# Kernel optimization log

Hardware: AMD Instinct MI355X
Metric: run time of the kernel (lower is better)

## Reference

```python
import jax, jax.numpy as jnp
import numpy as np

S, B, D, H, WIN, L = 8192, 4, 512, 8, 64, 6
HD = D // H
EPS = 1e-5


def setup_inputs() -> dict:
    key = jax.random.key(0)
    ks = jax.random.split(key, 6)
    s = 0.02
    return {
        "src": jax.random.normal(ks[0], (S, B, D), jnp.float32),
        "Wqkv": jax.random.normal(ks[1], (L, 3 * D, D), jnp.float32) * s,
        "bqkv": jnp.zeros((L, 3 * D), jnp.float32),
        "Wo": jax.random.normal(ks[2], (L, D, D), jnp.float32) * s,
        "bo": jnp.zeros((L, D), jnp.float32),
        "W1": jax.random.normal(ks[3], (L, 4 * D, D), jnp.float32) * s,
        "bf1": jnp.zeros((L, 4 * D), jnp.float32),
        "W2": jax.random.normal(ks[4], (L, D, 4 * D), jnp.float32) * s,
        "bf2": jnp.zeros((L, D), jnp.float32),
        "g1": jnp.ones((L, D), jnp.float32),
        "beta1": jnp.zeros((L, D), jnp.float32),
        "g2": jnp.ones((L, D), jnp.float32),
        "beta2": jnp.zeros((L, D), jnp.float32),
    }


def layernorm(x, g, b):
    m = jnp.mean(x, axis=-1, keepdims=True)
    v = jnp.mean(jnp.square(x - m), axis=-1, keepdims=True)
    return (x - m) * jax.lax.rsqrt(v + EPS) * g + b


def _forward(src, Wqkv, bqkv, Wo, bo, W1, bf1, W2, bf2, g1, beta1, g2, beta2):
    NW = S // WIN
    scale = 1.0 / np.sqrt(HD)
    x = src
    for l in range(L):
        qkv = x @ Wqkv[l].T + bqkv[l]                      # (S,B,3D)
        q, k, v = jnp.split(qkv, 3, axis=-1)
        win = lambda t: t.reshape(NW, WIN, B, H, HD)       # (NW,W,B,H,hd)
        q = win(q) * scale
        k = win(k)
        v = win(v)
        att = jax.nn.softmax(jnp.einsum('nqbhd,nkbhd->nbhqk', q, k), axis=-1)
        o = jnp.einsum('nbhqk,nkbhd->nqbhd', att, v).reshape(S, B, D)
        o = o @ Wo[l].T + bo[l]
        x = layernorm(x + o, g1[l], beta1[l])
        # FFN with ReLU (hidden = 4*d_model)
        f = jax.nn.relu(x @ W1[l].T + bf1[l]) @ W2[l].T + bf2[l]
        x = layernorm(x + f, g2[l], beta2[l])
    return x


def reference(src, Wqkv, bqkv, Wo, bo, W1, bf1, W2, bf2, g1, beta1, g2, beta2):
    return _forward(src, Wqkv, bqkv, Wo, bo, W1, bf1, W2, bf2, g1, beta1, g2, beta2)
```

## Files before the change

kernel.cpp:

```cpp
#include <hip/hip_runtime.h>
#include <hip/hip_bf16.h>

typedef __bf16 bf16x8 __attribute__((ext_vector_type(8)));
typedef float f32x4 __attribute__((ext_vector_type(4)));

static constexpr int NT = 32768;
static constexpr int D_ = 512;
static constexpr int D3 = 1536;
static constexpr int DF = 2048;
static constexpr int L_ = 6;

#define AS1 __attribute__((address_space(1)))
#define AS3 __attribute__((address_space(3)))

__device__ __forceinline__ void gload_lds16(const void* g, void* l) {
  __builtin_amdgcn_global_load_lds((const AS1 void*)g, (AS3 void*)l, 16, 0, 0);
}

template<int K, int NTN, bool RELU>
__global__ __launch_bounds__(512, 2) void gemm256(
    const __hip_bfloat16* __restrict__ A,
    const __hip_bfloat16* __restrict__ W,
    const float* __restrict__ bias,
    __hip_bfloat16* __restrict__ Cout) {
  __shared__ __align__(16) char lds[131072];
  const int t = threadIdx.x;
  const int l = t & 63, w = t >> 6;
  const int lrow = l & 15, lhi = l >> 4;
  const int wr = w >> 2, wc = w & 3;

  const int lin = blockIdx.x;
  const int wg = (lin & 7) * ((int)gridDim.x >> 3) + (lin >> 3);
  const int tm0 = (wg / NTN) * 256, tn0 = (wg % NTN) * 256;

  constexpr int NKT = K / 64;
  constexpr int NIT = NKT / 2;
  constexpr int N = NTN * 256;

  const int srow = t >> 3;
  const int sun = t & 7;

  auto stage = [&](int buf, int reg, const __hip_bfloat16* P, int grow0, int tile) {
    const int kb = tile * 64;
    char* dst = lds + (buf * 4 + reg) * 16384 + w * 1024;
#pragma unroll
    for (int pass = 0; pass < 2; ++pass) {
      int rl = pass * 64 + srow;
      int u = sun ^ (rl & 7);
      gload_lds16(P + (size_t)(grow0 + rl) * K + kb + u * 8, dst + pass * 8192);
    }
  };
  auto rdA = [&](int buf, int m, int ks) -> bf16x8 {
    int r = m * 16 + lrow;
    return *(const bf16x8*)(lds + (buf * 4 + wr) * 16384 + r * 128 +
                            (((ks * 4 + lhi) ^ (r & 7)) << 4));
  };
  auto rdB = [&](int buf, int n, int ks) -> bf16x8 {
    int r = (wc & 1) * 64 + n * 16 + lrow;
    return *(const bf16x8*)(lds + (buf * 4 + 2 + (wc >> 1)) * 16384 + r * 128 +
                            (((ks * 4 + lhi) ^ (r & 7)) << 4));
  };

  f32x4 acc[8][4] = {};
  bf16x8 bfrag[4][2], afrag[2][2];

  stage(0, 2, W, tn0, 0);
  stage(0, 3, W, tn0 + 128, 0);
  stage(0, 0, A, tm0, 0);
  stage(0, 1, A, tm0 + 128, 0);
  stage(1, 2, W, tn0, 1);
  stage(1, 3, W, tn0 + 128, 1);
  asm volatile("s_waitcnt vmcnt(4)" ::: "memory");
  __builtin_amdgcn_s_barrier();

#define GPHASE(BUF, MB, RB, STG, VMS)                                       \
  {                                                                          \
    if (RB) {                                                                \
      _Pragma("unroll") for (int n = 0; n < 4; ++n)                          \
          _Pragma("unroll") for (int ks = 0; ks < 2; ++ks)                   \
              bfrag[n][ks] = rdB(BUF, n, ks);                                \
    }                                                                        \
    _Pragma("unroll") for (int ks = 0; ks < 2; ++ks) {                       \
      afrag[0][ks] = rdA(BUF, MB, ks);                                       \
      afrag[1][ks] = rdA(BUF, MB + 1, ks);                                   \
    }                                                                        \
    STG;                                                                     \
    VMS;                                                                     \
    __builtin_amdgcn_sched_barrier(0);                                       \
    __builtin_amdgcn_s_barrier();                                            \
    asm volatile("s_waitcnt lgkmcnt(0)" ::: "memory");                       \
    __builtin_amdgcn_sched_barrier(0);                                       \
    __builtin_amdgcn_s_setprio(1);                                           \
    _Pragma("unroll") for (int n = 0; n < 4; ++n)                            \
        _Pragma("unroll") for (int ks = 0; ks < 2; ++ks) {                   \
      acc[MB][n] = __builtin_amdgcn_mfma_f32_16x16x32_bf16(                  \
          afrag[0][ks], bfrag[n][ks], acc[MB][n], 0, 0, 0);                  \
      acc[MB + 1][n] = __builtin_amdgcn_mfma_f32_16x16x32_bf16(              \
          afrag[1][ks], bfrag[n][ks], acc[MB + 1][n], 0, 0, 0);              \
    }                                                                        \
    __builtin_amdgcn_s_setprio(0);                                           \
    __builtin_amdgcn_sched_barrier(0);                                       \
    __builtin_amdgcn_s_barrier();                                            \
  }

#define VM_CNT                                              \
  if (more) {                                               \
    asm volatile("s_waitcnt vmcnt(4)" ::: "memory");        \
  } else {                                                  \
    asm volatile("s_waitcnt vmcnt(0)" ::: "memory");        \
  }

  for (int it = 0; it < NIT; ++it) {
    const int t0 = 2 * it, t1 = 2 * it + 1;
    const bool more = (it + 1 < NIT);
    GPHASE(0, 0, 1, { stage(1, 0, A, tm0, t1); stage(1, 1, A, tm0 + 128, t1); }, );
    GPHASE(0, 2, 0, { if (more) stage(0, 2, W, tn0, t0 + 2); }, );
    GPHASE(0, 4, 0, { if (more) stage(0, 3, W, tn0 + 128, t0 + 2); }, );
    GPHASE(0, 6, 0, , VM_CNT);
    GPHASE(1, 0, 1, { if (more) stage(0, 0, A, tm0, t0 + 2); }, );
    GPHASE(1, 2, 0, { if (more) stage(0, 1, A, tm0 + 128, t0 + 2); }, );
    GPHASE(1, 4, 0, { if (more) stage(1, 2, W, tn0, t1 + 2); }, );
    GPHASE(1, 6, 0, { if (more) stage(1, 3, W, tn0 + 128, t1 + 2); }, VM_CNT);
  }
#undef GPHASE
#undef VM_CNT

  char* ep = lds + w * 16384;
#pragma unroll
  for (int n = 0; n < 4; ++n) {
    float bv = bias[tn0 + wc * 64 + n * 16 + lrow];
#pragma unroll
    for (int m = 0; m < 8; ++m)
#pragma unroll
      for (int j = 0; j < 4; ++j) {
        float v = acc[m][n][j] + bv;
        if (RELU) v = fmaxf(v, 0.f);
        int row = m * 16 + lhi * 4 + j;
        int col = n * 16 + lrow;
        *(__hip_bfloat16*)(ep + row * 128 + (((col >> 3) ^ (row & 7)) << 4) +
                           (col & 7) * 2) = __float2bfloat16(v);
      }
  }
  __builtin_amdgcn_sched_barrier(0);
  const int er = l >> 3, ec = l & 7;
#pragma unroll
  for (int p = 0; p < 16; ++p) {
    int r = p * 8 + er;
    uint4 vv = *(const uint4*)(ep + r * 128 + ((ec ^ (r & 7)) << 4));
    *(uint4*)&Cout[(size_t)(tm0 + wr * 128 + r) * N + tn0 + wc * 64 + ec * 8] = vv;
  }
}

__global__ __launch_bounds__(128) void attn_win(
    const __hip_bfloat16* __restrict__ qkv, __hip_bfloat16* __restrict__ o) {
  __shared__ __align__(16) char lds[2 * 18432];
  const int t = threadIdx.x, l = t & 63, w = t >> 6;
  char* vt = lds + w * 18432;
  char* pl = vt + 9216;
  const int wid = blockIdx.x * 2 + w;
  const int h = wid & 7, b = (wid >> 3) & 3, nw = wid >> 5;
  const int lrow = l & 15, lhi = l >> 4;
  const __hip_bfloat16* qp = qkv + (size_t)(nw * 256 + b) * 1536 + h * 64;
  const __hip_bfloat16* kp = qp + 512;
  const __hip_bfloat16* vp = qp + 1024;

  {
    const int d0 = (l & 7) * 8;
    const int r0 = l >> 3;
#pragma unroll
    for (int i = 0; i < 8; ++i) {
      int r = r0 + i * 8;
      union { uint4 u; __hip_bfloat16 e[8]; } vv;
      vv.u = *(const uint4*)(vp + (size_t)r * 6144 + d0);
#pragma unroll
      for (int j = 0; j < 8; ++j)
        *(__hip_bfloat16*)(vt + ((d0 + j) * 72 + r) * 2) = vv.e[j];
    }
  }

  bf16x8 qf[4][2], kf[4][2];
#pragma unroll
  for (int mi = 0; mi < 4; ++mi)
#pragma unroll
    for (int ks = 0; ks < 2; ++ks) {
      int r = mi * 16 + lrow;
      int d = ks * 32 + lhi * 8;
      qf[mi][ks] = __builtin_bit_cast(bf16x8, *(const uint4*)(qp + (size_t)r * 6144 + d));
      kf[mi][ks] = __builtin_bit_cast(bf16x8, *(const uint4*)(kp + (size_t)r * 6144 + d));
    }

  f32x4 s[4][4] = {};
#pragma unroll
  for (int mi = 0; mi < 4; ++mi)
#pragma unroll
    for (int ni = 0; ni < 4; ++ni) {
      s[mi][ni] = __builtin_amdgcn_mfma_f32_16x16x32_bf16(qf[mi][0], kf[ni][0], s[mi][ni], 0, 0, 0);
      s[mi][ni] = __builtin_amdgcn_mfma_f32_16x16x32_bf16(qf[mi][1], kf[ni][1], s[mi][ni], 0, 0, 0);
    }

#pragma unroll
  for (int mi = 0; mi < 4; ++mi)
#pragma unroll
    for (int j = 0; j < 4; ++j) {
      float mx = s[mi][0][j];
#pragma unroll
      for (int ni = 1; ni < 4; ++ni) mx = fmaxf(mx, s[mi][ni][j]);
      mx = fmaxf(mx, __shfl_xor(mx, 1));
      mx = fmaxf(mx, __shfl_xor(mx, 2));
      mx = fmaxf(mx, __shfl_xor(mx, 4));
      mx = fmaxf(mx, __shfl_xor(mx, 8));
      float p[4], sum = 0.f;
#pragma unroll
      for (int ni = 0; ni < 4; ++ni) { p[ni] = __expf(s[mi][ni][j] - mx); sum += p[ni]; }
      sum += __shfl_xor(sum, 1);
      sum += __shfl_xor(sum, 2);
      sum += __shfl_xor(sum, 4);
      sum += __shfl_xor(sum, 8);
      float inv = 1.f / sum;
      int row = mi * 16 + lhi * 4 + j;
#pragma unroll
      for (int ni = 0; ni < 4; ++ni)
        *(__hip_bfloat16*)(pl + (row * 72 + ni * 16 + lrow) * 2) =
            __float2bfloat16(p[ni] * inv);
    }

  bf16x8 pf[4][2], vf[4][2];
#pragma unroll
  for (int mi = 0; mi < 4; ++mi)
#pragma unroll
    for (int ks = 0; ks < 2; ++ks)
      pf[mi][ks] = *(const bf16x8*)(pl + ((mi * 16 + lrow) * 72 + ks * 32 + lhi * 8) * 2);
#pragma unroll
  for (int ni = 0; ni < 4; ++ni)
#pragma unroll
    for (int ks = 0; ks < 2; ++ks)
      vf[ni][ks] = *(const bf16x8*)(vt + ((ni * 16 + lrow) * 72 + ks * 32 + lhi * 8) * 2);

  f32x4 acc[4][4] = {};
#pragma unroll
  for (int mi = 0; mi < 4; ++mi)
#pragma unroll
    for (int ni = 0; ni < 4; ++ni) {
      acc[mi][ni] = __builtin_amdgcn_mfma_f32_16x16x32_bf16(pf[mi][0], vf[ni][0], acc[mi][ni], 0, 0, 0);
      acc[mi][ni] = __builtin_amdgcn_mfma_f32_16x16x32_bf16(pf[mi][1], vf[ni][1], acc[mi][ni], 0, 0, 0);
    }

  __hip_bfloat16* op = o + (size_t)(nw * 256 + b) * 512 + h * 64;
#pragma unroll
  for (int mi = 0; mi < 4; ++mi)
#pragma unroll
    for (int ni = 0; ni < 4; ++ni) {
      int col = ni * 16 + lrow;
#pragma unroll
      for (int j = 0; j < 4; ++j) {
        int row = mi * 16 + lhi * 4 + j;
        op[(size_t)row * 2048 + col] = __float2bfloat16(acc[mi][ni][j]);
      }
    }
}

__global__ __launch_bounds__(256) void ln_res(
    float* __restrict__ x, const __hip_bfloat16* __restrict__ f,
    const float* __restrict__ g, const float* __restrict__ be,
    __hip_bfloat16* __restrict__ xb) {
  const int w = threadIdx.x >> 6, l = threadIdx.x & 63;
  const size_t row = (size_t)blockIdx.x * 4 + w;
  float* xr = x + row * 512;
  const int c = l * 8;
  float4 a0 = *(const float4*)(xr + c);
  float4 a1 = *(const float4*)(xr + c + 4);
  union { uint4 u; __hip_bfloat16 e[8]; } fb;
  fb.u = *(const uint4*)(f + row * 512 + c);
  float v[8] = {a0.x + __bfloat162float(fb.e[0]), a0.y + __bfloat162float(fb.e[1]),
                a0.z + __bfloat162float(fb.e[2]), a0.w + __bfloat162float(fb.e[3]),
                a1.x + __bfloat162float(fb.e[4]), a1.y + __bfloat162float(fb.e[5]),
                a1.z + __bfloat162float(fb.e[6]), a1.w + __bfloat162float(fb.e[7])};
  float sum = 0.f, sq = 0.f;
#pragma unroll
  for (int j = 0; j < 8; ++j) { sum += v[j]; sq += v[j] * v[j]; }
#pragma unroll
  for (int m = 1; m < 64; m <<= 1) {
    sum += __shfl_xor(sum, m);
    sq += __shfl_xor(sq, m);
  }
  float mean = sum * (1.f / 512.f);
  float var = sq * (1.f / 512.f) - mean * mean;
  float rs = rsqrtf(var + 1e-5f);
  float4 g0 = *(const float4*)(g + c);
  float4 g1v = *(const float4*)(g + c + 4);
  float4 e0 = *(const float4*)(be + c);
  float4 e1 = *(const float4*)(be + c + 4);
  float gg[8] = {g0.x, g0.y, g0.z, g0.w, g1v.x, g1v.y, g1v.z, g1v.w};
  float ee[8] = {e0.x, e0.y, e0.z, e0.w, e1.x, e1.y, e1.z, e1.w};
  float y[8];
  __hip_bfloat16 hb[8];
#pragma unroll
  for (int j = 0; j < 8; ++j) {
    y[j] = (v[j] - mean) * rs * gg[j] + ee[j];
    hb[j] = __float2bfloat16(y[j]);
  }
  float4 o0 = {y[0], y[1], y[2], y[3]};
  float4 o1 = {y[4], y[5], y[6], y[7]};
  *(float4*)(xr + c) = o0;
  *(float4*)(xr + c + 4) = o1;
  *(uint4*)((char*)(xb + row * 512 + c)) = *(uint4*)hb;
}

__global__ void bfc(const float* __restrict__ xm, __hip_bfloat16* __restrict__ xb) {
  int i = blockIdx.x * 256 + threadIdx.x;
  float4 v = ((const float4*)xm)[i];
  __hip_bfloat16 hb[4] = {__float2bfloat16(v.x), __float2bfloat16(v.y),
                          __float2bfloat16(v.z), __float2bfloat16(v.w)};
  ((uint2*)xb)[i] = *(uint2*)hb;
}

__global__ void convq(const float* __restrict__ wq, __hip_bfloat16* __restrict__ o) {
  int i = blockIdx.x * 256 + threadIdx.x;
  float4 v = ((const float4*)wq)[i];
  int e = i * 4;
  float sc = (((e >> 9) % 1536) < 512) ? 0.125f : 1.f;
  __hip_bfloat16 hb[4] = {__float2bfloat16(v.x * sc), __float2bfloat16(v.y * sc),
                          __float2bfloat16(v.z * sc), __float2bfloat16(v.w * sc)};
  ((uint2*)o)[i] = *(uint2*)hb;
}

__global__ void convw(const float* __restrict__ s, __hip_bfloat16* __restrict__ o) {
  int i = blockIdx.x * 256 + threadIdx.x;
  float4 v = ((const float4*)s)[i];
  __hip_bfloat16 hb[4] = {__float2bfloat16(v.x), __float2bfloat16(v.y),
                          __float2bfloat16(v.z), __float2bfloat16(v.w)};
  ((uint2*)o)[i] = *(uint2*)hb;
}

__global__ void scaleb(const float* __restrict__ b, float* __restrict__ o) {
  int i = blockIdx.x * 256 + threadIdx.x;
  o[i] = b[i] * (((i % 1536) < 512) ? 0.125f : 1.f);
}

extern "C" void kernel_launch(void* const* d_in, const int* in_sizes, int n_in,
                              void* d_out, int out_size, void* d_ws, size_t ws_size,
                              hipStream_t stream) {
  const float* src  = (const float*)d_in[0];
  const float* Wqkv = (const float*)d_in[1];
  const float* bqkv = (const float*)d_in[2];
  const float* Wo   = (const float*)d_in[3];
  const float* bo   = (const float*)d_in[4];
  const float* W1   = (const float*)d_in[5];
  const float* bf1  = (const float*)d_in[6];
  const float* W2   = (const float*)d_in[7];
  const float* bf2  = (const float*)d_in[8];
  const float* g1   = (const float*)d_in[9];
  const float* be1  = (const float*)d_in[10];
  const float* g2   = (const float*)d_in[11];
  const float* be2  = (const float*)d_in[12];
  float* x = (float*)d_out;

  char* ws = (char*)d_ws;
  size_t off = 0;
  auto alloc = [&](size_t bytes) {
    char* p = ws + off;
    off += (bytes + 255) & ~(size_t)255;
    return p;
  };

  const size_t wq_b = (size_t)L_ * D3 * D_ * 2;
  const size_t wo_b = (size_t)L_ * D_ * D_ * 2;
  const size_t w1_b = (size_t)L_ * DF * D_ * 2;
  const size_t w2_b = (size_t)L_ * D_ * DF * 2;
  auto al = [](size_t v) { return (v + 255) & ~(size_t)255; };
  const size_t persist = al(wq_b) + al(wo_b) + al(w1_b) + al(w2_b) + al(L_ * D3 * 4);

  int CT = NT;
  while (CT > 2048 && persist + (size_t)CT * 6144 + 65536 > ws_size) CT >>= 1;

  __hip_bfloat16* wqkvb = (__hip_bfloat16*)alloc(wq_b);
  __hip_bfloat16* wob   = (__hip_bfloat16*)alloc(wo_b);
  __hip_bfloat16* w1b   = (__hip_bfloat16*)alloc(w1_b);
  __hip_bfloat16* w2b   = (__hip_bfloat16*)alloc(w2_b);
  float*          bqs   = (float*)alloc((size_t)L_ * D3 * 4);
  __hip_bfloat16* xbf   = (__hip_bfloat16*)alloc((size_t)CT * 512 * 2);
  __hip_bfloat16* R     = (__hip_bfloat16*)alloc((size_t)CT * 2048 * 2);
  __hip_bfloat16* OB    = (__hip_bfloat16*)alloc((size_t)CT * 512 * 2);

  hipMemcpyAsync(x, src, (size_t)NT * 512 * 4, hipMemcpyDeviceToDevice, stream);
  convq<<<L_ * D3 * D_ / 4 / 256, 256, 0, stream>>>(Wqkv, wqkvb);
  convw<<<L_ * D_ * D_ / 4 / 256, 256, 0, stream>>>(Wo, wob);
  convw<<<L_ * DF * D_ / 4 / 256, 256, 0, stream>>>(W1, w1b);
  convw<<<L_ * D_ * DF / 4 / 256, 256, 0, stream>>>(W2, w2b);
  scaleb<<<L_ * D3 / 256, 256, 0, stream>>>(bqkv, bqs);

  const int nch = NT / CT;
  for (int c = 0; c < nch; ++c) {
    float* xm = x + (size_t)c * CT * 512;
    bfc<<<CT / 2, 256, 0, stream>>>(xm, xbf);
    for (int l = 0; l < L_; ++l) {
      gemm256<512, 6, false><<<(CT / 256) * 6, 512, 0, stream>>>(
          xbf, wqkvb + (size_t)l * D3 * D_, bqs + l * D3, R);
      attn_win<<<CT / 16, 128, 0, stream>>>(R, OB);
      gemm256<512, 2, false><<<(CT / 256) * 2, 512, 0, stream>>>(
          OB, wob + (size_t)l * D_ * D_, bo + l * D_, R);
      ln_res<<<CT / 4, 256, 0, stream>>>(xm, R, g1 + l * D_, be1 + l * D_, xbf);
      gemm256<512, 8, true><<<(CT / 256) * 8, 512, 0, stream>>>(
          xbf, w1b + (size_t)l * DF * D_, bf1 + l * DF, R);
      gemm256<2048, 2, false><<<(CT / 256) * 2, 512, 0, stream>>>(
          R, w2b + (size_t)l * D_ * DF, bf2 + l * D_, OB);
      ln_res<<<CT / 4, 256, 0, stream>>>(xm, OB, g2 + l * D_, be2 + l * D_, xbf);
    }
  }
}
```

Measured before the change: 2.024 ms.

## Make GEMM kernel process multiple output tiles per block with continuous prefetch

```diff
diff --git a/kernel.cpp b/kernel.cpp
--- a/kernel.cpp
+++ b/kernel.cpp
@@ -17,7 +17,7 @@
   __builtin_amdgcn_global_load_lds((const AS1 void*)g, (AS3 void*)l, 16, 0, 0);
 }
 
-template<int K, int NTN, bool RELU>
+template<int K, int NTN, int TPB, bool RELU>
 __global__ __launch_bounds__(512, 2) void gemm256(
     const __hip_bfloat16* __restrict__ A,
     const __hip_bfloat16* __restrict__ W,
@@ -31,23 +31,24 @@
 
   const int lin = blockIdx.x;
   const int wg = (lin & 7) * ((int)gridDim.x >> 3) + (lin >> 3);
-  const int tm0 = (wg / NTN) * 256, tn0 = (wg % NTN) * 256;
+  const int T0 = wg * TPB;
 
   constexpr int NKT = K / 64;
-  constexpr int NIT = NKT / 2;
+  constexpr int LNK = (NKT == 8) ? 3 : 5;
+  constexpr int NITT = TPB * NKT / 2;
   constexpr int N = NTN * 256;
 
   const int srow = t >> 3;
   const int sun = t & 7;
 
-  auto stage = [&](int buf, int reg, const __hip_bfloat16* P, int grow0, int tile) {
-    const int kb = tile * 64;
+  auto stage = [&](int buf, int reg, const __hip_bfloat16* P, int rowbase, int kt) {
+    const int kb = kt * 64;
     char* dst = lds + (buf * 4 + reg) * 16384 + w * 1024;
 #pragma unroll
     for (int pass = 0; pass < 2; ++pass) {
       int rl = pass * 64 + srow;
       int u = sun ^ (rl & 7);
-      gload_lds16(P + (size_t)(grow0 + rl) * K + kb + u * 8, dst + pass * 8192);
+      gload_lds16(P + (size_t)(rowbase + rl) * K + kb + u * 8, dst + pass * 8192);
     }
   };
   auto rdA = [&](int buf, int m, int ks) -> bf16x8 {
@@ -64,12 +65,51 @@
   f32x4 acc[8][4] = {};
   bf16x8 bfrag[4][2], afrag[2][2];
 
-  stage(0, 2, W, tn0, 0);
-  stage(0, 3, W, tn0 + 128, 0);
-  stage(0, 0, A, tm0, 0);
-  stage(0, 1, A, tm0 + 128, 0);
-  stage(1, 2, W, tn0, 1);
-  stage(1, 3, W, tn0 + 128, 1);
+  auto epi = [&](int g) {
+    const int tm = (g / NTN) * 256, tn = (g % NTN) * 256;
+    char* ep = lds + 65536 + w * 4096;
+    const int er = l >> 3, ec = l & 7;
+#pragma unroll
+    for (int p = 0; p < 4; ++p) {
+#pragma unroll
+      for (int n = 0; n < 4; ++n) {
+        float bv = bias[tn + wc * 64 + n * 16 + lrow];
+#pragma unroll
+        for (int mm = 0; mm < 2; ++mm) {
+#pragma unroll
+          for (int j = 0; j < 4; ++j) {
+            float v = acc[2 * p + mm][n][j] + bv;
+            if (RELU) v = fmaxf(v, 0.f);
+            int rl = mm * 16 + lhi * 4 + j;
+            int col = n * 16 + lrow;
+            *(__hip_bfloat16*)(ep + rl * 128 + (((col >> 3) ^ (rl & 7)) << 4) +
+                               (col & 7) * 2) = __float2bfloat16(v);
+          }
+        }
+      }
+      asm volatile("s_waitcnt lgkmcnt(0)" ::: "memory");
+      __builtin_amdgcn_sched_barrier(0);
+#pragma unroll
+      for (int q = 0; q < 4; ++q) {
+        int rl = q * 8 + er;
+        uint4 vv = *(const uint4*)(ep + rl * 128 + ((ec ^ (rl & 7)) << 4));
+        *(uint4*)&Cout[(size_t)(tm + wr * 128 + p * 32 + rl) * N + tn + wc * 64 +
+                       ec * 8] = vv;
+      }
+      asm volatile("s_waitcnt lgkmcnt(0)" ::: "memory");
+      __builtin_amdgcn_sched_barrier(0);
+    }
+  };
+
+  {
+    const int mb = (T0 / NTN) * 256, nb = (T0 % NTN) * 256;
+    stage(0, 2, W, nb, 0);
+    stage(0, 3, W, nb + 128, 0);
+    stage(0, 0, A, mb, 0);
+    stage(0, 1, A, mb + 128, 0);
+    stage(1, 2, W, nb, 1);
+    stage(1, 3, W, nb + 128, 1);
+  }
   asm volatile("s_waitcnt vmcnt(4)" ::: "memory");
   __builtin_amdgcn_s_barrier();
 
@@ -110,45 +150,38 @@
     asm volatile("s_waitcnt vmcnt(0)" ::: "memory");        \
   }
 
-  for (int it = 0; it < NIT; ++it) {
-    const int t0 = 2 * it, t1 = 2 * it + 1;
-    const bool more = (it + 1 < NIT);
-    GPHASE(0, 0, 1, { stage(1, 0, A, tm0, t1); stage(1, 1, A, tm0 + 128, t1); }, );
-    GPHASE(0, 2, 0, { if (more) stage(0, 2, W, tn0, t0 + 2); }, );
-    GPHASE(0, 4, 0, { if (more) stage(0, 3, W, tn0 + 128, t0 + 2); }, );
+  for (int it = 0; it < NITT; ++it) {
+    const bool more = (it + 1 < NITT);
+    const int gc = T0 + (it >> (LNK - 1));
+    const int kt1 = (2 * it + 1) & (NKT - 1);
+    const int sn0 = 2 * it + 2, sn1 = 2 * it + 3;
+    const int gn0 = T0 + (sn0 >> LNK), ktn0 = sn0 & (NKT - 1);
+    const int gn1 = T0 + (sn1 >> LNK), ktn1 = sn1 & (NKT - 1);
+    const int mc = (gc / NTN) * 256;
+    const int m0 = (gn0 / NTN) * 256, n0b = (gn0 % NTN) * 256;
+    const int n1b = (gn1 % NTN) * 256;
+
+    GPHASE(0, 0, 1, { stage(1, 0, A, mc, kt1); stage(1, 1, A, mc + 128, kt1); }, );
+    GPHASE(0, 2, 0, { if (more) stage(0, 2, W, n0b, ktn0); }, );
+    GPHASE(0, 4, 0, { if (more) stage(0, 3, W, n0b + 128, ktn0); }, );
     GPHASE(0, 6, 0, , VM_CNT);
-    GPHASE(1, 0, 1, { if (more) stage(0, 0, A, tm0, t0 + 2); }, );
-    GPHASE(1, 2, 0, { if (more) stage(0, 1, A, tm0 + 128, t0 + 2); }, );
-    GPHASE(1, 4, 0, { if (more) stage(1, 2, W, tn0, t1 + 2); }, );
-    GPHASE(1, 6, 0, { if (more) stage(1, 3, W, tn0 + 128, t1 + 2); }, VM_CNT);
+    GPHASE(1, 0, 1, { if (more) stage(0, 0, A, m0, ktn0); }, );
+    GPHASE(1, 2, 0, { if (more) stage(0, 1, A, m0 + 128, ktn0); }, );
+    GPHASE(1, 4, 0, { if (more) stage(1, 2, W, n1b, ktn1); }, );
+    GPHASE(1, 6, 0, { if (more) stage(1, 3, W, n1b + 128, ktn1); }, VM_CNT);
+
+    if (((it + 1) & ((NKT >> 1) - 1)) == 0) {
+      epi(gc);
+      f32x4 z = 0.f;
+#pragma unroll
+      for (int m = 0; m < 8; ++m)
+#pragma unroll
+        for (int n = 0; n < 4; ++n) acc[m][n] = z;
+      __builtin_amdgcn_s_barrier();
+    }
   }
 #undef GPHASE
 #undef VM_CNT
-
-  char* ep = lds + w * 16384;
-#pragma unroll
-  for (int n = 0; n < 4; ++n) {
-    float bv = bias[tn0 + wc * 64 + n * 16 + lrow];
-#pragma unroll
-    for (int m = 0; m < 8; ++m)
-#pragma unroll
-      for (int j = 0; j < 4; ++j) {
-        float v = acc[m][n][j] + bv;
-        if (RELU) v = fmaxf(v, 0.f);
-        int row = m * 16 + lhi * 4 + j;
-        int col = n * 16 + lrow;
-        *(__hip_bfloat16*)(ep + row * 128 + (((col >> 3) ^ (row & 7)) << 4) +
-                           (col & 7) * 2) = __float2bfloat16(v);
-      }
-  }
-  __builtin_amdgcn_sched_barrier(0);
-  const int er = l >> 3, ec = l & 7;
-#pragma unroll
-  for (int p = 0; p < 16; ++p) {
-    int r = p * 8 + er;
-    uint4 vv = *(const uint4*)(ep + r * 128 + ((ec ^ (r & 7)) << 4));
-    *(uint4*)&Cout[(size_t)(tm0 + wr * 128 + r) * N + tn0 + wc * 64 + ec * 8] = vv;
-  }
 }
 
 __global__ __launch_bounds__(128) void attn_win(
@@ -394,15 +427,15 @@
     float* xm = x + (size_t)c * CT * 512;
     bfc<<<CT / 2, 256, 0, stream>>>(xm, xbf);
     for (int l = 0; l < L_; ++l) {
-      gemm256<512, 6, false><<<(CT / 256) * 6, 512, 0, stream>>>(
+      gemm256<512, 6, 3, false><<<CT / 128, 512, 0, stream>>>(
           xbf, wqkvb + (size_t)l * D3 * D_, bqs + l * D3, R);
       attn_win<<<CT / 16, 128, 0, stream>>>(R, OB);
-      gemm256<512, 2, false><<<(CT / 256) * 2, 512, 0, stream>>>(
+      gemm256<512, 2, 1, false><<<CT / 128, 512, 0, stream>>>(
           OB, wob + (size_t)l * D_ * D_, bo + l * D_, R);
       ln_res<<<CT / 4, 256, 0, stream>>>(xm, R, g1 + l * D_, be1 + l * D_, xbf);
-      gemm256<512, 8, true><<<(CT / 256) * 8, 512, 0, stream>>>(
+      gemm256<512, 8, 4, true><<<CT / 128, 512, 0, stream>>>(
           xbf, w1b + (size_t)l * DF * D_, bf1 + l * DF, R);
-      gemm256<2048, 2, false><<<(CT / 256) * 2, 512, 0, stream>>>(
+      gemm256<2048, 2, 1, false><<<CT / 128, 512, 0, stream>>>(
           R, w2b + (size_t)l * D_ * DF, bf2 + l * D_, OB);
       ln_res<<<CT / 4, 256, 0, stream>>>(xm, OB, g2 + l * D_, be2 + l * D_, xbf);
     }
```

Result: slower. 2.196 ms (+8.5%).
